# Optimization experiments

Hardware: AMD Instinct MI355X
Metric: run time of the kernel (lower is better)

Reference implementation:

```python
import jax, jax.numpy as jnp
import numpy as np

EPS = 1e-5

def layer_norm(x, g, b):
    m = jnp.mean(x, axis=-1, keepdims=True)
    v = jnp.var(x, axis=-1, keepdims=True)
    return (x - m) / jnp.sqrt(v + EPS) * g + b


def setup_inputs() -> dict:
    key = jax.random.key(0)
    ks = jax.random.split(key, 12)
    B, L, D = 4, 4096, 512
    DF = 2 * D  # dim * dim_ff_scale
    inp = {
        "x": jax.random.normal(ks[0], (B, L, D), dtype=jnp.float32),
        "hidden_real": jax.random.normal(ks[1], (B, D), dtype=jnp.float32),
        "hidden_imag": jax.random.normal(ks[2], (B, D), dtype=jnp.float32),
        # SpiralConv complex params (real/imag parts), as torch.randn cfloat
        "phazor_re": jax.random.normal(ks[3], (D,), dtype=jnp.float32),
        "phazor_im": jax.random.normal(ks[4], (D,), dtype=jnp.float32),
        "pinit_re": jax.random.normal(ks[5], (D,), dtype=jnp.float32),
        "pinit_im": jax.random.normal(ks[6], (D,), dtype=jnp.float32),
        # shared LayerNorm params
        "ln_g": jnp.ones((D,), dtype=jnp.float32),
        "ln_b": jnp.zeros((D,), dtype=jnp.float32),
        # FFN params
        "w1": jax.random.normal(ks[7], (D, DF), dtype=jnp.float32) * (1.0 / np.sqrt(D)),
        "b1": jnp.zeros((DF,), dtype=jnp.float32),
        "w2": jax.random.normal(ks[8], (DF, D), dtype=jnp.float32) * (1.0 / np.sqrt(DF)),
        "b2": jnp.zeros((D,), dtype=jnp.float32),
    }
    return inp


def reference(x, hidden_real, hidden_imag, phazor_re, phazor_im,
              pinit_re, pinit_im, ln_g, ln_b, w1, b1, w2, b2):
    B, L, D = x.shape
    p = jax.lax.complex(phazor_re, phazor_im)
    pinit = jax.lax.complex(pinit_re, pinit_im)
    hidden_last = jax.lax.complex(hidden_real, hidden_imag)

    # phazor = p/|p| * exp(-|p|)  (unit direction, decaying magnitude)
    absp = jnp.abs(p)
    phazor = p / absp * jnp.exp(-absp)

    # phazor_progression[t, d] = phazor[d] ** t
    t = jnp.arange(L, dtype=jnp.float32)
    prog = jnp.exp(t[:, None] * jnp.log(phazor)[None, :])  # [L, D] complex
    filt = prog * pinit[None, :]                            # [L, D]

    x_res = x
    xn = layer_norm(x, ln_g, ln_b)

    # FFT long convolution along sequence, zero-padded to 2L (linear conv)
    filt_fft = jnp.fft.fft(filt, n=2 * L, axis=0)           # [2L, D]
    x_fft = jnp.fft.fft(xn, n=2 * L, axis=1)                # [B, 2L, D]
    conv = jnp.fft.ifft(filt_fft[None, :, :] * x_fft, axis=1)[:, :L, :]

    hidden = conv + hidden_last[:, None, :] * prog[None, :, :] * phazor[None, None, :]

    y = hidden.real + x_res
    yn = layer_norm(y, ln_g, ln_b)
    h = yn @ w1 + b1
    h = h * jax.nn.sigmoid(h)  # SiLU; dropout=0 (eval) is identity
    out = h @ w2 + b2 + y
    return out, hidden
```

## Files before the change

kernel.cpp:

```cpp
#include <hip/hip_runtime.h>
#include <hip/hip_bf16.h>
#include <math.h>

#define BB 4
#define LL 4096
#define DD 512
#define DF 1024
#define CHUNKS 128
#define LC 32
#define HALF_ROWS 8192

typedef __bf16 bf16x8 __attribute__((ext_vector_type(8)));
typedef float f32x4 __attribute__((ext_vector_type(4)));

__device__ inline void get_phazor(const float* __restrict__ pre, const float* __restrict__ pim,
                                  int d, float& ar, float& ai) {
    float pr = pre[d], pi = pim[d];
    float ab = sqrtf(pr * pr + pi * pi);
    float sc = expf(-ab) / ab;
    ar = pr * sc;
    ai = pi * sc;
}

__global__ __launch_bounds__(256) void k_wt(const float* __restrict__ w1, const float* __restrict__ w2,
                                            __bf16* __restrict__ w1t, __bf16* __restrict__ w2t) {
    __shared__ float tile[32][33];
    const float* src;
    __bf16* dst;
    int R, C;
    if (blockIdx.y == 0) { src = w1; dst = w1t; R = DD; C = DF; }
    else                 { src = w2; dst = w2t; R = DF; C = DD; }
    int ntx = C / 32;
    int c0 = (blockIdx.x % ntx) * 32, r0 = (blockIdx.x / ntx) * 32;
    int tx = threadIdx.x & 31, ty = threadIdx.x >> 5;
#pragma unroll
    for (int i = 0; i < 32; i += 8)
        tile[ty + i][tx] = src[(size_t)(r0 + ty + i) * C + c0 + tx];
    __syncthreads();
#pragma unroll
    for (int i = 0; i < 32; i += 8)
        dst[(size_t)(c0 + ty + i) * R + r0 + tx] = (__bf16)tile[tx][ty + i];
}

__global__ __launch_bounds__(256) void k_xstats(const float* __restrict__ x, float* __restrict__ xstats) {
    int wave = threadIdx.x >> 6, lane = threadIdx.x & 63;
    size_t row = (size_t)blockIdx.x * 4 + wave;
    const float4* xr = reinterpret_cast<const float4*>(x + row * DD) + lane * 2;
    float4 a = xr[0], b = xr[1];
    float s = a.x + a.y + a.z + a.w + b.x + b.y + b.z + b.w;
    float q = a.x * a.x + a.y * a.y + a.z * a.z + a.w * a.w +
              b.x * b.x + b.y * b.y + b.z * b.z + b.w * b.w;
#pragma unroll
    for (int off = 32; off; off >>= 1) {
        s += __shfl_down(s, off);
        q += __shfl_down(q, off);
    }
    if (lane == 0) {
        float m = s * (1.0f / DD);
        float v = q * (1.0f / DD) - m * m;
        xstats[row * 2 + 0] = m;
        xstats[row * 2 + 1] = rsqrtf(v + 1e-5f);
    }
}

__global__ __launch_bounds__(512) void k_scan_partial(
    const float* __restrict__ x, const float* __restrict__ xstats,
    const float* __restrict__ pre, const float* __restrict__ pim,
    const float* __restrict__ pinr, const float* __restrict__ pini,
    const float* __restrict__ g, const float* __restrict__ bvec,
    float* __restrict__ carry) {
    int d = threadIdx.x;
    int c = blockIdx.x % CHUNKS, b = blockIdx.x / CHUNKS;
    float ar, ai;
    get_phazor(pre, pim, d, ar, ai);
    float pr = pinr[d], pi = pini[d];
    float gd = g[d], bd = bvec[d];
    float hr = 0.f, hi = 0.f;
    int l0 = c * LC;
    const float* xp = x + ((size_t)b * LL + l0) * DD + d;
    const float* st = xstats + ((size_t)b * LL + l0) * 2;
    for (int i = 0; i < LC; i++) {
        float m = st[2 * i], r = st[2 * i + 1];
        float xn = (xp[(size_t)i * DD] - m) * r * gd + bd;
        float ur = pr * xn, ui = pi * xn;
        float t = ar * hr - ai * hi + ur;
        hi = ar * hi + ai * hr + ui;
        hr = t;
    }
    size_t idx = ((size_t)blockIdx.x * DD + d) * 2;
    carry[idx] = hr;
    carry[idx + 1] = hi;
}

__global__ __launch_bounds__(64) void k_chunk_scan(
    const float* __restrict__ hr0, const float* __restrict__ hi0,
    const float* __restrict__ pre, const float* __restrict__ pim,
    float* __restrict__ carry) {
    int b = blockIdx.x >> 3;
    int d = ((blockIdx.x & 7) << 6) + threadIdx.x;
    float ar, ai;
    get_phazor(pre, pim, d, ar, ai);
    float sr = ar, si = ai;
#pragma unroll
    for (int p = 1; p < LC; p <<= 1) {
        float t = sr * sr - si * si;
        si = 2.f * sr * si;
        sr = t;
    }
    float cr = hr0[b * DD + d], ci = hi0[b * DD + d];
    float2* cp = reinterpret_cast<float2*>(carry);
    for (int k = 0; k < CHUNKS; k++) {
        size_t idx = ((size_t)b * CHUNKS + k) * DD + d;
        float2 t2 = cp[idx];
        cp[idx] = make_float2(cr, ci);
        float t = sr * cr - si * ci + t2.x;
        ci = sr * ci + si * cr + t2.y;
        cr = t;
    }
}

template <int MODE>
__global__ __launch_bounds__(512) void k_scan_out(
    const float* __restrict__ x, const float* __restrict__ xstats,
    const float* __restrict__ pre, const float* __restrict__ pim,
    const float* __restrict__ pinr, const float* __restrict__ pini,
    const float* __restrict__ g, const float* __restrict__ bvec,
    const float* __restrict__ carry_in,
    float* __restrict__ out_y, float* __restrict__ hid) {
    int d = threadIdx.x;
    int c = blockIdx.x % CHUNKS, b = blockIdx.x / CHUNKS;
    float ar, ai;
    get_phazor(pre, pim, d, ar, ai);
    float pr = pinr[d], pi = pini[d];
    float gd = g[d], bd = bvec[d];
    size_t cidx = ((size_t)blockIdx.x * DD + d) * 2;
    float hr = carry_in[cidx], hi = carry_in[cidx + 1];
    int l0 = c * LC;
    const float* xp = x + ((size_t)b * LL + l0) * DD + d;
    const float* st = xstats + ((size_t)b * LL + l0) * 2;
    for (int i = 0; i < LC; i++) {
        float m = st[2 * i], r = st[2 * i + 1];
        float xv = xp[(size_t)i * DD];
        float xn = (xv - m) * r * gd + bd;
        float ur = pr * xn, ui = pi * xn;
        float t = ar * hr - ai * hi + ur;
        hi = ar * hi + ai * hr + ui;
        hr = t;
        size_t row = (size_t)b * LL + l0 + i;
        if constexpr (MODE == 0) {
            out_y[row * DD + d] = hr + xv;
        } else if constexpr (MODE == 1) {
            hid[row * DD + d] = hr;
        } else if constexpr (MODE == 2) {
            reinterpret_cast<float2*>(hid)[row * DD + d] = make_float2(hr, hi);
        } else {
            out_y[row * DD + d] = hr + xv;
            hid[row * DD + d] = hr;
        }
    }
}

__global__ __launch_bounds__(256) void k_ynorm(const float* __restrict__ y,
                                               const float* __restrict__ g, const float* __restrict__ bvec,
                                               __bf16* __restrict__ yn) {
    int wave = threadIdx.x >> 6, lane = threadIdx.x & 63;
    size_t row = (size_t)blockIdx.x * 4 + wave;
    const float4* yr = reinterpret_cast<const float4*>(y + row * DD) + lane * 2;
    float4 a = yr[0], b = yr[1];
    float s = a.x + a.y + a.z + a.w + b.x + b.y + b.z + b.w;
    float q = a.x * a.x + a.y * a.y + a.z * a.z + a.w * a.w +
              b.x * b.x + b.y * b.y + b.z * b.z + b.w * b.w;
#pragma unroll
    for (int off = 32; off; off >>= 1) {
        s += __shfl_xor(s, off);
        q += __shfl_xor(q, off);
    }
    float m = s * (1.0f / DD);
    float r = rsqrtf(q * (1.0f / DD) - m * m + 1e-5f);
    int dbase = lane * 8;
    const float4* gp = reinterpret_cast<const float4*>(g + dbase);
    const float4* bp = reinterpret_cast<const float4*>(bvec + dbase);
    float4 g0 = gp[0], g1 = gp[1], b0 = bp[0], b1 = bp[1];
    bf16x8 o;
    o[0] = (__bf16)((a.x - m) * r * g0.x + b0.x);
    o[1] = (__bf16)((a.y - m) * r * g0.y + b0.y);
    o[2] = (__bf16)((a.z - m) * r * g0.z + b0.z);
    o[3] = (__bf16)((a.w - m) * r * g0.w + b0.w);
    o[4] = (__bf16)((b.x - m) * r * g1.x + b1.x);
    o[5] = (__bf16)((b.y - m) * r * g1.y + b1.y);
    o[6] = (__bf16)((b.z - m) * r * g1.z + b1.z);
    o[7] = (__bf16)((b.w - m) * r * g1.w + b1.w);
    *reinterpret_cast<bf16x8*>(yn + row * DD + dbase) = o;
}

template <int BM, int BN, int KDIM, int NDIM, int EPI>
__global__ __launch_bounds__(512) void k_gemm(
    const __bf16* __restrict__ A, const __bf16* __restrict__ Bt,
    const float* __restrict__ bias, const float* __restrict__ yadd,
    float* __restrict__ outf, __bf16* __restrict__ outb) {
    __shared__ __align__(16) __bf16 As[2][BM * 64];
    __shared__ __align__(16) __bf16 Bs[2][BN * 64];
    constexpr int NT = NDIM / BN;
    constexpr int MR = BM / 32;
    constexpr int NR = BN / 64;
    constexpr int LPT = BM / 64 + BN / 64;
    int nwg = gridDim.x;
    int bid = blockIdx.x;
    int swz = (bid & 7) * (nwg >> 3) + (bid >> 3);
    int m0 = (swz / NT) * BM;
    int n0 = (swz % NT) * BN;
    int tid = threadIdx.x;
    int wid = tid >> 6, lane = tid & 63;

    f32x4 acc[MR][NR] = {};

    int wm = (wid >> 2) * (BM / 2), wn = (wid & 3) * (BN / 4);
    int fr = lane & 15;
    int qbase = lane >> 4;

    auto stage = [&](int buf, int k0) {
#pragma unroll
        for (int i = 0; i < BM / 64; i++) {
            int c = tid + i * 512;
            int row = c >> 3, kq = c & 7;
            int kqg = kq ^ (row & 7);
            const __bf16* ga = A + (size_t)(m0 + row) * KDIM + k0 + kqg * 8;
            __bf16* la = &As[buf][(size_t)(i * 512 + wid * 64) * 8];
            __builtin_amdgcn_global_load_lds((const __attribute__((address_space(1))) unsigned int*)ga,
                                             (__attribute__((address_space(3))) unsigned int*)la, 16, 0, 0);
        }
#pragma unroll
        for (int i = 0; i < BN / 64; i++) {
            int c = tid + i * 512;
            int row = c >> 3, kq = c & 7;
            int kqg = kq ^ (row & 7);
            const __bf16* gb = Bt + (size_t)(n0 + row) * KDIM + k0 + kqg * 8;
            __bf16* lb = &Bs[buf][(size_t)(i * 512 + wid * 64) * 8];
            __builtin_amdgcn_global_load_lds((const __attribute__((address_space(1))) unsigned int*)gb,
                                             (__attribute__((address_space(3))) unsigned int*)lb, 16, 0, 0);
        }
    };

    auto compute = [&](int buf) {
#pragma unroll
        for (int ks = 0; ks < 2; ks++) {
            int q = ks * 4 + qbase;
            bf16x8 af[MR], bfv[NR];
#pragma unroll
            for (int mi = 0; mi < MR; mi++) {
                int R = wm + mi * 16 + fr;
                af[mi] = *reinterpret_cast<const bf16x8*>(&As[buf][R * 64 + ((q ^ (R & 7)) << 3)]);
            }
#pragma unroll
            for (int ni = 0; ni < NR; ni++) {
                int R = wn + ni * 16 + fr;
                bfv[ni] = *reinterpret_cast<const bf16x8*>(&Bs[buf][R * 64 + ((q ^ (R & 7)) << 3)]);
            }
            __builtin_amdgcn_s_setprio(1);
#pragma unroll
            for (int mi = 0; mi < MR; mi++)
#pragma unroll
                for (int ni = 0; ni < NR; ni++)
                    acc[mi][ni] = __builtin_amdgcn_mfma_f32_16x16x32_bf16(af[mi], bfv[ni],
                                                                          acc[mi][ni], 0, 0, 0);
            __builtin_amdgcn_s_setprio(0);
        }
    };

    stage(0, 0);
    int cur = 0;
    for (int k0 = 64; k0 < KDIM; k0 += 64) {
        stage(cur ^ 1, k0);
        asm volatile("s_waitcnt vmcnt(%0)" ::"i"(LPT) : "memory");
        __builtin_amdgcn_s_barrier();
        compute(cur);
        __builtin_amdgcn_s_barrier();
        cur ^= 1;
    }
    asm volatile("s_waitcnt vmcnt(0)" ::: "memory");
    __builtin_amdgcn_s_barrier();
    compute(cur);

    int orow = (lane >> 4) * 4;
    int ocol = lane & 15;
#pragma unroll
    for (int mi = 0; mi < MR; mi++) {
#pragma unroll
        for (int ni = 0; ni < NR; ni++) {
            int gr = m0 + wm + mi * 16 + orow;
            int gc = n0 + wn + ni * 16 + ocol;
            float bv = bias[gc];
#pragma unroll
            for (int j = 0; j < 4; j++) {
                float v = acc[mi][ni][j] + bv;
                size_t idx = (size_t)(gr + j) * NDIM + gc;
                if constexpr (EPI == 1) {
                    float sv = v / (1.0f + __expf(-v));
                    outb[idx] = (__bf16)sv;
                } else {
                    outf[idx] = v + yadd[idx];
                }
            }
        }
    }
}

extern "C" void kernel_launch(void* const* d_in, const int* in_sizes, int n_in,
                              void* d_out, int out_size, void* d_ws, size_t ws_size,
                              hipStream_t stream) {
    const float* x = (const float*)d_in[0];
    const float* hr0 = (const float*)d_in[1];
    const float* hi0 = (const float*)d_in[2];
    const float* pre = (const float*)d_in[3];
    const float* pim = (const float*)d_in[4];
    const float* pinr = (const float*)d_in[5];
    const float* pini = (const float*)d_in[6];
    const float* lng = (const float*)d_in[7];
    const float* lnb = (const float*)d_in[8];
    const float* w1 = (const float*)d_in[9];
    const float* b1 = (const float*)d_in[10];
    const float* w2 = (const float*)d_in[11];
    const float* b2 = (const float*)d_in[12];

    const size_t n = (size_t)BB * LL * DD;
    float* outp = (float*)d_out;
    char* hidbase = (char*)d_out + n * 4;
    float* hidp = (float*)hidbase;
    bool interleaved = (out_size >= (int)(3 * n));

    char* ws = (char*)d_ws;
    float* xstats = (float*)ws;      ws += (size_t)BB * LL * 2 * 4;
    float* carry = (float*)ws;       ws += (size_t)BB * CHUNKS * DD * 8;
    __bf16* w1t = (__bf16*)ws;       ws += (size_t)DD * DF * 2;
    __bf16* w2t = (__bf16*)ws;       ws += (size_t)DF * DD * 2;
    char* ws_big = ws;
    const size_t SMALL = ((size_t)128 << 10) + ((size_t)2 << 20) + ((size_t)2 << 20);
    const size_t NEED_FULL = SMALL + ((size_t)48 << 20);
    const size_t NEED_HALF = SMALL + ((size_t)24 << 20);

    k_wt<<<dim3((DD / 32) * (DF / 32), 2), 256, 0, stream>>>(w1, w2, w1t, w2t);
    k_xstats<<<(BB * LL) / 4, 256, 0, stream>>>(x, xstats);
    k_scan_partial<<<BB * CHUNKS, 512, 0, stream>>>(x, xstats, pre, pim, pinr, pini, lng, lnb, carry);
    k_chunk_scan<<<BB * 8, 64, 0, stream>>>(hr0, hi0, pre, pim, carry);

    if (!interleaved && ws_size >= NEED_FULL) {
        __bf16* yn = (__bf16*)ws_big;
        __bf16* h1 = (__bf16*)(ws_big + ((size_t)16 << 20));
        k_scan_out<3><<<BB * CHUNKS, 512, 0, stream>>>(x, xstats, pre, pim, pinr, pini, lng, lnb,
                                                       carry, outp, hidp);
        k_ynorm<<<(BB * LL) / 4, 256, 0, stream>>>(outp, lng, lnb, yn);
        k_gemm<256, 256, DD, DF, 1><<<(BB * LL / 256) * (DF / 256), 512, 0, stream>>>(
            yn, w1t, b1, nullptr, nullptr, h1);
        k_gemm<128, 256, DF, DD, 2><<<(BB * LL / 128) * (DD / 256), 512, 0, stream>>>(
            h1, w2t, b2, outp, outp, nullptr);
    } else if (!interleaved && ws_size >= NEED_HALF) {
        __bf16* yn_h = (__bf16*)ws_big;
        __bf16* h1_h = (__bf16*)(ws_big + ((size_t)8 << 20));
        k_scan_out<3><<<BB * CHUNKS, 512, 0, stream>>>(x, xstats, pre, pim, pinr, pini, lng, lnb,
                                                       carry, outp, hidp);
        for (int h = 0; h < 2; h++) {
            float* yh = outp + (size_t)h * HALF_ROWS * DD;
            k_ynorm<<<HALF_ROWS / 4, 256, 0, stream>>>(yh, lng, lnb, yn_h);
            k_gemm<256, 256, DD, DF, 1><<<(HALF_ROWS / 256) * (DF / 256), 512, 0, stream>>>(
                yn_h, w1t, b1, nullptr, nullptr, h1_h);
            k_gemm<128, 256, DF, DD, 2><<<(HALF_ROWS / 128) * (DD / 256), 512, 0, stream>>>(
                h1_h, w2t, b2, yh, yh, nullptr);
        }
    } else {
        __bf16* yn_h = (__bf16*)hidbase;
        __bf16* h1_h = (__bf16*)(hidbase + ((size_t)8 << 20));
        k_scan_out<0><<<BB * CHUNKS, 512, 0, stream>>>(x, xstats, pre, pim, pinr, pini, lng, lnb,
                                                       carry, outp, nullptr);
        for (int h = 0; h < 2; h++) {
            float* yh = outp + (size_t)h * HALF_ROWS * DD;
            k_ynorm<<<HALF_ROWS / 4, 256, 0, stream>>>(yh, lng, lnb, yn_h);
            k_gemm<256, 256, DD, DF, 1><<<(HALF_ROWS / 256) * (DF / 256), 512, 0, stream>>>(
                yn_h, w1t, b1, nullptr, nullptr, h1_h);
            k_gemm<128, 256, DF, DD, 2><<<(HALF_ROWS / 128) * (DD / 256), 512, 0, stream>>>(
                h1_h, w2t, b2, yh, yh, nullptr);
        }
        if (interleaved) {
            k_scan_out<2><<<BB * CHUNKS, 512, 0, stream>>>(x, xstats, pre, pim, pinr, pini, lng, lnb,
                                                           carry, nullptr, hidp);
        } else {
            k_scan_out<1><<<BB * CHUNKS, 512, 0, stream>>>(x, xstats, pre, pim, pinr, pini, lng, lnb,
                                                           carry, nullptr, hidp);
        }
    }
}
```

Before: 114.6 us.

## Fuse output LayerNorm into scan output kernel and halve scan chunk length

Adds a scan-output mode that keeps y in registers, reduces per-row mean and variance across the block with shuffles and shared memory, and writes the bf16 normalized y directly. This removes the separate ynorm pass, which re-read y from global memory. Chunk count doubles (length 16) for more parallelism, and chunk_scan becomes one 512-thread block per batch. The carry buffer now aliases the h1 workspace, and the workspace thresholds are recomputed. The trade-off is a longer serial carry loop in chunk_scan and more register use.

```diff
diff --git a/kernel.cpp b/kernel.cpp
--- a/kernel.cpp
+++ b/kernel.cpp
@@ -6,8 +6,8 @@
 #define LL 4096
 #define DD 512
 #define DF 1024
-#define CHUNKS 128
-#define LC 32
+#define CHUNKS 256
+#define LC 16
 #define HALF_ROWS 8192
 
 typedef __bf16 bf16x8 __attribute__((ext_vector_type(8)));
@@ -79,6 +79,7 @@
     int l0 = c * LC;
     const float* xp = x + ((size_t)b * LL + l0) * DD + d;
     const float* st = xstats + ((size_t)b * LL + l0) * 2;
+#pragma unroll
     for (int i = 0; i < LC; i++) {
         float m = st[2 * i], r = st[2 * i + 1];
         float xn = (xp[(size_t)i * DD] - m) * r * gd + bd;
@@ -92,12 +93,12 @@
     carry[idx + 1] = hi;
 }
 
-__global__ __launch_bounds__(64) void k_chunk_scan(
+__global__ __launch_bounds__(512) void k_chunk_scan(
     const float* __restrict__ hr0, const float* __restrict__ hi0,
     const float* __restrict__ pre, const float* __restrict__ pim,
     float* __restrict__ carry) {
-    int b = blockIdx.x >> 3;
-    int d = ((blockIdx.x & 7) << 6) + threadIdx.x;
+    int b = blockIdx.x;
+    int d = threadIdx.x;
     float ar, ai;
     get_phazor(pre, pim, d, ar, ai);
     float sr = ar, si = ai;
@@ -126,7 +127,7 @@
     const float* __restrict__ pinr, const float* __restrict__ pini,
     const float* __restrict__ g, const float* __restrict__ bvec,
     const float* __restrict__ carry_in,
-    float* __restrict__ out_y, float* __restrict__ hid) {
+    float* __restrict__ out_y, float* __restrict__ hid, __bf16* __restrict__ yn) {
     int d = threadIdx.x;
     int c = blockIdx.x % CHUNKS, b = blockIdx.x / CHUNKS;
     float ar, ai;
@@ -138,6 +139,13 @@
     int l0 = c * LC;
     const float* xp = x + ((size_t)b * LL + l0) * DD + d;
     const float* st = xstats + ((size_t)b * LL + l0) * 2;
+
+    float yreg[LC];
+    __shared__ float sm[LC][8][2];
+    __shared__ float2 stats[LC];
+    int w = d >> 6, lane = d & 63;
+
+#pragma unroll
     for (int i = 0; i < LC; i++) {
         float m = st[2 * i], r = st[2 * i + 1];
         float xv = xp[(size_t)i * DD];
@@ -153,9 +161,44 @@
             hid[row * DD + d] = hr;
         } else if constexpr (MODE == 2) {
             reinterpret_cast<float2*>(hid)[row * DD + d] = make_float2(hr, hi);
-        } else {
+        } else if constexpr (MODE == 3) {
             out_y[row * DD + d] = hr + xv;
             hid[row * DD + d] = hr;
+        } else {
+            float yv = hr + xv;
+            out_y[row * DD + d] = yv;
+            hid[row * DD + d] = hr;
+            yreg[i] = yv;
+            float s = yv, q = yv * yv;
+#pragma unroll
+            for (int off = 32; off; off >>= 1) {
+                s += __shfl_xor(s, off);
+                q += __shfl_xor(q, off);
+            }
+            if (lane == 0) { sm[i][w][0] = s; sm[i][w][1] = q; }
+        }
+    }
+
+    if constexpr (MODE == 4) {
+        __syncthreads();
+        if (d < LC * 8) {
+            int r = d >> 3, w2 = d & 7;
+            float s = sm[r][w2][0], q = sm[r][w2][1];
+            s += __shfl_down(s, 4); q += __shfl_down(q, 4);
+            s += __shfl_down(s, 2); q += __shfl_down(q, 2);
+            s += __shfl_down(s, 1); q += __shfl_down(q, 1);
+            if (w2 == 0) {
+                float m = s * (1.0f / DD);
+                float v = q * (1.0f / DD) - m * m;
+                stats[r] = make_float2(m, rsqrtf(v + 1e-5f));
+            }
+        }
+        __syncthreads();
+#pragma unroll
+        for (int i = 0; i < LC; i++) {
+            float2 s2 = stats[i];
+            size_t row = (size_t)b * LL + l0 + i;
+            yn[row * DD + d] = (__bf16)((yreg[i] - s2.x) * s2.y * gd + bd);
         }
     }
 }
@@ -323,6 +366,7 @@
     const float* b2 = (const float*)d_in[12];
 
     const size_t n = (size_t)BB * LL * DD;
+    const size_t MB1 = 1ull << 20;
     float* outp = (float*)d_out;
     char* hidbase = (char*)d_out + n * 4;
     float* hidp = (float*)hidbase;
@@ -330,34 +374,40 @@
 
     char* ws = (char*)d_ws;
     float* xstats = (float*)ws;      ws += (size_t)BB * LL * 2 * 4;
-    float* carry = (float*)ws;       ws += (size_t)BB * CHUNKS * DD * 8;
     __bf16* w1t = (__bf16*)ws;       ws += (size_t)DD * DF * 2;
     __bf16* w2t = (__bf16*)ws;       ws += (size_t)DF * DD * 2;
     char* ws_big = ws;
-    const size_t SMALL = ((size_t)128 << 10) + ((size_t)2 << 20) + ((size_t)2 << 20);
-    const size_t NEED_FULL = SMALL + ((size_t)48 << 20);
-    const size_t NEED_HALF = SMALL + ((size_t)24 << 20);
+    const size_t CARRYB = (size_t)BB * CHUNKS * DD * 8;
+    const size_t SMALL = ((size_t)128 << 10) + 2 * MB1;
+    const size_t NEED_FULL = SMALL + 48 * MB1;
+    const size_t NEED_HALF = SMALL + CARRYB + 24 * MB1;
+    const size_t NEED_MIN = SMALL + CARRYB;
 
     k_wt<<<dim3((DD / 32) * (DF / 32), 2), 256, 0, stream>>>(w1, w2, w1t, w2t);
     k_xstats<<<(BB * LL) / 4, 256, 0, stream>>>(x, xstats);
-    k_scan_partial<<<BB * CHUNKS, 512, 0, stream>>>(x, xstats, pre, pim, pinr, pini, lng, lnb, carry);
-    k_chunk_scan<<<BB * 8, 64, 0, stream>>>(hr0, hi0, pre, pim, carry);
 
     if (!interleaved && ws_size >= NEED_FULL) {
         __bf16* yn = (__bf16*)ws_big;
-        __bf16* h1 = (__bf16*)(ws_big + ((size_t)16 << 20));
-        k_scan_out<3><<<BB * CHUNKS, 512, 0, stream>>>(x, xstats, pre, pim, pinr, pini, lng, lnb,
-                                                       carry, outp, hidp);
-        k_ynorm<<<(BB * LL) / 4, 256, 0, stream>>>(outp, lng, lnb, yn);
+        __bf16* h1 = (__bf16*)(ws_big + 16 * MB1);
+        float* carry = (float*)(ws_big + 16 * MB1);
+        k_scan_partial<<<BB * CHUNKS, 512, 0, stream>>>(x, xstats, pre, pim, pinr, pini, lng, lnb,
+                                                        carry);
+        k_chunk_scan<<<BB, 512, 0, stream>>>(hr0, hi0, pre, pim, carry);
+        k_scan_out<4><<<BB * CHUNKS, 512, 0, stream>>>(x, xstats, pre, pim, pinr, pini, lng, lnb,
+                                                       carry, outp, hidp, yn);
         k_gemm<256, 256, DD, DF, 1><<<(BB * LL / 256) * (DF / 256), 512, 0, stream>>>(
             yn, w1t, b1, nullptr, nullptr, h1);
         k_gemm<128, 256, DF, DD, 2><<<(BB * LL / 128) * (DD / 256), 512, 0, stream>>>(
             h1, w2t, b2, outp, outp, nullptr);
     } else if (!interleaved && ws_size >= NEED_HALF) {
-        __bf16* yn_h = (__bf16*)ws_big;
-        __bf16* h1_h = (__bf16*)(ws_big + ((size_t)8 << 20));
+        float* carry = (float*)ws_big;
+        __bf16* yn_h = (__bf16*)(ws_big + CARRYB);
+        __bf16* h1_h = (__bf16*)(ws_big + CARRYB + 8 * MB1);
+        k_scan_partial<<<BB * CHUNKS, 512, 0, stream>>>(x, xstats, pre, pim, pinr, pini, lng, lnb,
+                                                        carry);
+        k_chunk_scan<<<BB, 512, 0, stream>>>(hr0, hi0, pre, pim, carry);
         k_scan_out<3><<<BB * CHUNKS, 512, 0, stream>>>(x, xstats, pre, pim, pinr, pini, lng, lnb,
-                                                       carry, outp, hidp);
+                                                       carry, outp, hidp, nullptr);
         for (int h = 0; h < 2; h++) {
             float* yh = outp + (size_t)h * HALF_ROWS * DD;
             k_ynorm<<<HALF_ROWS / 4, 256, 0, stream>>>(yh, lng, lnb, yn_h);
@@ -367,10 +417,14 @@
                 h1_h, w2t, b2, yh, yh, nullptr);
         }
     } else {
+        float* carry = (float*)ws_big;
         __bf16* yn_h = (__bf16*)hidbase;
-        __bf16* h1_h = (__bf16*)(hidbase + ((size_t)8 << 20));
+        __bf16* h1_h = (__bf16*)(hidbase + 8 * MB1);
+        k_scan_partial<<<BB * CHUNKS, 512, 0, stream>>>(x, xstats, pre, pim, pinr, pini, lng, lnb,
+                                                        carry);
+        k_chunk_scan<<<BB, 512, 0, stream>>>(hr0, hi0, pre, pim, carry);
         k_scan_out<0><<<BB * CHUNKS, 512, 0, stream>>>(x, xstats, pre, pim, pinr, pini, lng, lnb,
-                                                       carry, outp, nullptr);
+                                                       carry, outp, nullptr, nullptr);
         for (int h = 0; h < 2; h++) {
             float* yh = outp + (size_t)h * HALF_ROWS * DD;
             k_ynorm<<<HALF_ROWS / 4, 256, 0, stream>>>(yh, lng, lnb, yn_h);
@@ -381,10 +435,10 @@
         }
         if (interleaved) {
             k_scan_out<2><<<BB * CHUNKS, 512, 0, stream>>>(x, xstats, pre, pim, pinr, pini, lng, lnb,
-                                                           carry, nullptr, hidp);
+                                                           carry, nullptr, hidp, nullptr);
         } else {
             k_scan_out<1><<<BB * CHUNKS, 512, 0, stream>>>(x, xstats, pre, pim, pinr, pini, lng, lnb,
-                                                           carry, nullptr, hidp);
-        }
-    }
-}
+                                                           carry, nullptr, hidp, nullptr);
+        }
+    }
+}
```

Result: slower. 137.1 us (+19.6%).

## Parallelize chunk carry scan with two-level hierarchical scan across 512 threads

Applied to the files above, without the earlier changes.

The sequential 128-step carry scan per (batch, channel) is split into 8 groups of 16 chunks, each handled by its own wavefront. Group totals are combined through shared memory using the phazor raised to the 512th power, and each group then rescans its chunks from the resulting start value. This shortens the serial dependency chain and raises occupancy of a tiny latency-bound kernel, at the cost of reading the carry buffer twice. Workspace size constants are also rewritten with a named MB constant.

```diff
diff --git a/kernel.cpp b/kernel.cpp
--- a/kernel.cpp
+++ b/kernel.cpp
@@ -92,30 +92,57 @@
     carry[idx + 1] = hi;
 }
 
-__global__ __launch_bounds__(64) void k_chunk_scan(
+__global__ __launch_bounds__(512) void k_chunk_scan(
     const float* __restrict__ hr0, const float* __restrict__ hi0,
     const float* __restrict__ pre, const float* __restrict__ pim,
     float* __restrict__ carry) {
     int b = blockIdx.x >> 3;
-    int d = ((blockIdx.x & 7) << 6) + threadIdx.x;
+    int dgroup = blockIdx.x & 7;
+    int dlocal = threadIdx.x & 63;
+    int kt = threadIdx.x >> 6;
+    int d = dgroup * 64 + dlocal;
+    __shared__ float2 smc[8][64];
     float ar, ai;
     get_phazor(pre, pim, d, ar, ai);
-    float sr = ar, si = ai;
-#pragma unroll
-    for (int p = 1; p < LC; p <<= 1) {
-        float t = sr * sr - si * si;
-        si = 2.f * sr * si;
-        sr = t;
-    }
-    float cr = hr0[b * DD + d], ci = hi0[b * DD + d];
+    float Ar = ar, Ai = ai;
+#pragma unroll
+    for (int p = 1; p < LC; p <<= 1) { float t = Ar * Ar - Ai * Ai; Ai = 2.f * Ar * Ai; Ar = t; }
+    float Gr = Ar, Gi = Ai;
+#pragma unroll
+    for (int p = 0; p < 4; p++) { float t = Gr * Gr - Gi * Gi; Gi = 2.f * Gr * Gi; Gr = t; }
     float2* cp = reinterpret_cast<float2*>(carry);
-    for (int k = 0; k < CHUNKS; k++) {
-        size_t idx = ((size_t)b * CHUNKS + k) * DD + d;
-        float2 t2 = cp[idx];
-        cp[idx] = make_float2(cr, ci);
-        float t = sr * cr - si * ci + t2.x;
-        ci = sr * ci + si * cr + t2.y;
+    size_t base = ((size_t)b * CHUNKS + kt * 16) * DD + d;
+    float cr = 0.f, ci = 0.f;
+#pragma unroll
+    for (int i = 0; i < 16; i++) {
+        float2 p2 = cp[base + (size_t)i * DD];
+        float t = Ar * cr - Ai * ci + p2.x;
+        ci = Ar * ci + Ai * cr + p2.y;
         cr = t;
+    }
+    smc[kt][dlocal] = make_float2(cr, ci);
+    __syncthreads();
+    if (kt == 0) {
+        float Sr = hr0[b * DD + d], Si = hi0[b * DD + d];
+#pragma unroll
+        for (int j = 0; j < 8; j++) {
+            float2 t2 = smc[j][dlocal];
+            smc[j][dlocal] = make_float2(Sr, Si);
+            float t = Gr * Sr - Gi * Si + t2.x;
+            Si = Gr * Si + Gi * Sr + t2.y;
+            Sr = t;
+        }
+    }
+    __syncthreads();
+    float2 s0 = smc[kt][dlocal];
+    float Sr = s0.x, Si = s0.y;
+#pragma unroll
+    for (int i = 0; i < 16; i++) {
+        float2 p2 = cp[base + (size_t)i * DD];
+        cp[base + (size_t)i * DD] = make_float2(Sr, Si);
+        float t = Ar * Sr - Ai * Si + p2.x;
+        Si = Ar * Si + Ai * Sr + p2.y;
+        Sr = t;
     }
 }
 
@@ -323,6 +350,7 @@
     const float* b2 = (const float*)d_in[12];
 
     const size_t n = (size_t)BB * LL * DD;
+    const size_t MB1 = 1ull << 20;
     float* outp = (float*)d_out;
     char* hidbase = (char*)d_out + n * 4;
     float* hidp = (float*)hidbase;
@@ -334,18 +362,18 @@
     __bf16* w1t = (__bf16*)ws;       ws += (size_t)DD * DF * 2;
     __bf16* w2t = (__bf16*)ws;       ws += (size_t)DF * DD * 2;
     char* ws_big = ws;
-    const size_t SMALL = ((size_t)128 << 10) + ((size_t)2 << 20) + ((size_t)2 << 20);
-    const size_t NEED_FULL = SMALL + ((size_t)48 << 20);
-    const size_t NEED_HALF = SMALL + ((size_t)24 << 20);
+    const size_t SMALL = ((size_t)128 << 10) + 4 * MB1;
+    const size_t NEED_FULL = SMALL + 48 * MB1;
+    const size_t NEED_HALF = SMALL + 24 * MB1;
 
     k_wt<<<dim3((DD / 32) * (DF / 32), 2), 256, 0, stream>>>(w1, w2, w1t, w2t);
     k_xstats<<<(BB * LL) / 4, 256, 0, stream>>>(x, xstats);
     k_scan_partial<<<BB * CHUNKS, 512, 0, stream>>>(x, xstats, pre, pim, pinr, pini, lng, lnb, carry);
-    k_chunk_scan<<<BB * 8, 64, 0, stream>>>(hr0, hi0, pre, pim, carry);
+    k_chunk_scan<<<BB * 8, 512, 0, stream>>>(hr0, hi0, pre, pim, carry);
 
     if (!interleaved && ws_size >= NEED_FULL) {
         __bf16* yn = (__bf16*)ws_big;
-        __bf16* h1 = (__bf16*)(ws_big + ((size_t)16 << 20));
+        __bf16* h1 = (__bf16*)(ws_big + 16 * MB1);
         k_scan_out<3><<<BB * CHUNKS, 512, 0, stream>>>(x, xstats, pre, pim, pinr, pini, lng, lnb,
                                                        carry, outp, hidp);
         k_ynorm<<<(BB * LL) / 4, 256, 0, stream>>>(outp, lng, lnb, yn);
@@ -355,7 +383,7 @@
             h1, w2t, b2, outp, outp, nullptr);
     } else if (!interleaved && ws_size >= NEED_HALF) {
         __bf16* yn_h = (__bf16*)ws_big;
-        __bf16* h1_h = (__bf16*)(ws_big + ((size_t)8 << 20));
+        __bf16* h1_h = (__bf16*)(ws_big + 8 * MB1);
         k_scan_out<3><<<BB * CHUNKS, 512, 0, stream>>>(x, xstats, pre, pim, pinr, pini, lng, lnb,
                                                        carry, outp, hidp);
         for (int h = 0; h < 2; h++) {
@@ -368,7 +396,7 @@
         }
     } else {
         __bf16* yn_h = (__bf16*)hidbase;
-        __bf16* h1_h = (__bf16*)(hidbase + ((size_t)8 << 20));
+        __bf16* h1_h = (__bf16*)(hidbase + 8 * MB1);
         k_scan_out<0><<<BB * CHUNKS, 512, 0, stream>>>(x, xstats, pre, pim, pinr, pini, lng, lnb,
                                                        carry, outp, nullptr);
         for (int h = 0; h < 2; h++) {
```

Result: faster. 110.7 us (-3.5%).
